# Kernel optimization log

Measured on AMD Instinct MI355X. Metric: run time of the kernel, lower is better.

## Reference

```python
import jax, jax.numpy as jnp
import numpy as np

EMB_DIM = 256
N_EGO = 8192
N_SIDE = 8192
TOP_K = 16


def setup_inputs() -> dict:
    key = jax.random.key(0)
    ks = jax.random.split(key, 9)
    s = 1.0 / np.sqrt(EMB_DIM)
    return {
        "ego_emb": jax.random.normal(ks[0], (N_EGO, EMB_DIM), jnp.float32),
        "side_emb": jax.random.normal(ks[1], (N_SIDE, EMB_DIM), jnp.float32),
        "rel_emb": jax.random.normal(ks[2], (N_SIDE, EMB_DIM), jnp.float32),
        "Wq": jax.random.uniform(ks[3], (EMB_DIM, EMB_DIM), jnp.float32, -s, s),
        "bq": jax.random.uniform(ks[4], (EMB_DIM,), jnp.float32, -s, s),
        "Wk": jax.random.uniform(ks[5], (EMB_DIM, EMB_DIM), jnp.float32, -s, s),
        "bk": jax.random.uniform(ks[6], (EMB_DIM,), jnp.float32, -s, s),
        "Wv": jax.random.uniform(ks[7], (EMB_DIM, EMB_DIM), jnp.float32, -s, s),
        "bv": jax.random.uniform(ks[8], (EMB_DIM,), jnp.float32, -s, s),
    }


def reference(ego_emb, side_emb, rel_emb, Wq, bq, Wk, bk, Wv, bv):
    # Linear projections (torch nn.Linear: x @ W.T + b)
    q = ego_emb @ Wq.T + bq                      # [N_ego, d]
    k = (side_emb * rel_emb) @ Wk.T + bk         # [N_side, d]
    v = side_emb @ Wv.T + bv                     # [N_side, d]

    scale = jnp.sqrt(jnp.asarray(EMB_DIM, q.dtype))
    attn_scores = (q @ k.T) / scale              # [N_ego, N_side] dense

    k_value = min(TOP_K, attn_scores.shape[-1])
    topk_scores, topk_indices = jax.lax.top_k(attn_scores, k_value)  # [N_ego, K]
    attn_weights = jax.nn.softmax(topk_scores, axis=-1)              # [N_ego, K]

    topk_v = v[topk_indices]                     # gather -> [N_ego, K, d]
    aggregated = jnp.sum(topk_v * attn_weights[..., None], axis=1)   # [N_ego, d]
    return aggregated
```

## Files before the change

### kernel.cpp

```cpp
#include <hip/hip_runtime.h>
#include <hip/hip_bf16.h>


#define EMB 256
#define NEGO 8192
#define NSIDE 8192
#define TOPKK 16
#define NSPLIT 8
#define SPLITLEN (NSIDE / NSPLIT)
#define BM 128
#define BN 32
#define NGRP (SPLITLEN / BN)
#define CAP 8
#define RESCORE 20

typedef _Float16 f16x8 __attribute__((ext_vector_type(8)));
typedef float f32x16 __attribute__((ext_vector_type(16)));

#define NEG_BIG (-3.402823466e38f)

__device__ __forceinline__ void gload_lds16(const _Float16* g, _Float16* l) {
    __builtin_amdgcn_global_load_lds((const __attribute__((address_space(1))) void*)g,
                                     (__attribute__((address_space(3))) void*)l, 16, 0, 0);
}

__device__ __forceinline__ void split8(const float* xv, f16x8& hi, f16x8& lo) {
#pragma unroll
    for (int j = 0; j < 8; ++j) {
        float x = xv[j];
        _Float16 h = (_Float16)x;
        hi[j] = h;
        lo[j] = (_Float16)(x - (float)h);
    }
}

__device__ __forceinline__ unsigned packkey(float s, unsigned gid) {
    unsigned b = __float_as_uint(s);
    b = ((int)b >= 0) ? (b | 0x80000000u) : ~b;
    return (b & 0xFFFFE000u) | (gid ^ 0x1FFFu);
}

__global__ __launch_bounds__(256, 1) void proj_kernel(
    const float* __restrict__ ego, const float* __restrict__ side, const float* __restrict__ rel,
    const float* __restrict__ Wq, const float* __restrict__ bq,
    const float* __restrict__ Wk, const float* __restrict__ bk,
    const float* __restrict__ Wv, const float* __restrict__ bv,
    _Float16* __restrict__ qh, _Float16* __restrict__ ql,
    _Float16* __restrict__ kh, _Float16* __restrict__ kl,
    float* __restrict__ vout)
{
    __shared__ __align__(16) _Float16 Wh[64 * 256];
    __shared__ __align__(16) _Float16 Wl[64 * 256];

    const int z = blockIdx.y;
    const float* X; const float* W; const float* bias;
    if (z == 0)      { X = ego;  W = Wq; bias = bq; }
    else if (z == 1) { X = side; W = Wk; bias = bk; }
    else             { X = side; W = Wv; bias = bv; }

    const int tid = threadIdx.x, lane = tid & 63, wave = tid >> 6;
    const int hk = lane >> 5, r = lane & 31;
    const int arow = blockIdx.x * BM + wave * 32 + r;

    f16x8 ah[16], al[16];
#pragma unroll
    for (int kst = 0; kst < 16; ++kst) {
        float xv[8];
        const float* p = X + arow * EMB + kst * 16 + hk * 8;
        const float4 x0 = *(const float4*)p;
        const float4 x1 = *(const float4*)(p + 4);
        xv[0]=x0.x; xv[1]=x0.y; xv[2]=x0.z; xv[3]=x0.w;
        xv[4]=x1.x; xv[5]=x1.y; xv[6]=x1.z; xv[7]=x1.w;
        if (z == 1) {
            const float* pr = rel + arow * EMB + kst * 16 + hk * 8;
            const float4 r0 = *(const float4*)pr;
            const float4 r1 = *(const float4*)(pr + 4);
            xv[0]*=r0.x; xv[1]*=r0.y; xv[2]*=r0.z; xv[3]*=r0.w;
            xv[4]*=r1.x; xv[5]*=r1.y; xv[6]*=r1.z; xv[7]*=r1.w;
        }
        split8(xv, ah[kst], al[kst]);
    }

    for (int nt = 0; nt < 4; ++nt) {
        __syncthreads();
#pragma unroll
        for (int i = 0; i < 8; ++i) {
            const int rowi = wave * 16 + i * 2 + hk;
            const int c = r;
            const float* wp = W + (nt * 64 + rowi) * EMB + ((c ^ (rowi & 31)) << 3);
            float xv[8];
            const float4 w0 = *(const float4*)wp;
            const float4 w1 = *(const float4*)(wp + 4);
            xv[0]=w0.x; xv[1]=w0.y; xv[2]=w0.z; xv[3]=w0.w;
            xv[4]=w1.x; xv[5]=w1.y; xv[6]=w1.z; xv[7]=w1.w;
            f16x8 h8, l8;
            split8(xv, h8, l8);
            *(f16x8*)&Wh[rowi * 256 + c * 8] = h8;
            *(f16x8*)&Wl[rowi * 256 + c * 8] = l8;
        }
        __syncthreads();

        f32x16 acc0 = {}, acc1 = {};
#pragma unroll
        for (int kst = 0; kst < 16; ++kst) {
            const int cc = kst * 2 + hk;
            const f16x8 bh0 = *(const f16x8*)&Wh[r * 256 + ((cc ^ r) << 3)];
            const f16x8 bl0 = *(const f16x8*)&Wl[r * 256 + ((cc ^ r) << 3)];
            const f16x8 bh1 = *(const f16x8*)&Wh[(32 + r) * 256 + ((cc ^ r) << 3)];
            const f16x8 bl1 = *(const f16x8*)&Wl[(32 + r) * 256 + ((cc ^ r) << 3)];
            acc0 = __builtin_amdgcn_mfma_f32_32x32x16_f16(ah[kst], bh0, acc0, 0, 0, 0);
            acc0 = __builtin_amdgcn_mfma_f32_32x32x16_f16(al[kst], bh0, acc0, 0, 0, 0);
            acc0 = __builtin_amdgcn_mfma_f32_32x32x16_f16(ah[kst], bl0, acc0, 0, 0, 0);
            acc1 = __builtin_amdgcn_mfma_f32_32x32x16_f16(ah[kst], bh1, acc1, 0, 0, 0);
            acc1 = __builtin_amdgcn_mfma_f32_32x32x16_f16(al[kst], bh1, acc1, 0, 0, 0);
            acc1 = __builtin_amdgcn_mfma_f32_32x32x16_f16(ah[kst], bl1, acc1, 0, 0, 0);
        }

#pragma unroll
        for (int reg = 0; reg < 16; ++reg) {
            const int crow = (reg & 3) + 8 * (reg >> 2) + 4 * hk;
            const int grow = blockIdx.x * BM + wave * 32 + crow;
            const int col0 = nt * 64 + r;
            const int col1 = nt * 64 + 32 + r;
            const float v0 = acc0[reg] + bias[col0];
            const float v1 = acc1[reg] + bias[col1];
            if (z < 2) {
                _Float16* oh = (z == 0) ? qh : kh;
                _Float16* ol = (z == 0) ? ql : kl;
                _Float16 h0 = (_Float16)v0;
                oh[grow * EMB + col0] = h0;
                ol[grow * EMB + col0] = (_Float16)(v0 - (float)h0);
                _Float16 h1 = (_Float16)v1;
                oh[grow * EMB + col1] = h1;
                ol[grow * EMB + col1] = (_Float16)(v1 - (float)h1);
            } else {
                vout[grow * EMB + col0] = v0;
                vout[grow * EMB + col1] = v1;
            }
        }
    }
}

__global__ __launch_bounds__(256, 2) void scores_topk_kernel(
    const _Float16* __restrict__ qh,
    const _Float16* __restrict__ kh,
    unsigned* __restrict__ part)
{
    __shared__ __align__(16) _Float16 Bh[2 * BN * 256];
    __shared__ unsigned stk[(CAP + 1) * 256];

    const int tid = threadIdx.x, lane = tid & 63, wave = tid >> 6;
    const int hk = lane >> 5, r = lane & 31;
    const int split = blockIdx.x & 7;
    const int bx = blockIdx.x >> 3;
    const int qbase = bx * BM + wave * 32;
    const int rowoff0 = 4 * hk;
    const int gidbase = split * SPLITLEN;

    unsigned tk[16];
    unsigned curmin = 0u;

    f16x8 ah[16];
#pragma unroll
    for (int kst = 0; kst < 16; ++kst) {
        ah[kst] = *(const f16x8*)(qh + (qbase + r) * EMB + kst * 16 + hk * 8);
    }

    auto minTree = [&]() {
        unsigned m0 = min(tk[0], tk[1]),  m1 = min(tk[2], tk[3]);
        unsigned m2 = min(tk[4], tk[5]),  m3 = min(tk[6], tk[7]);
        unsigned m4 = min(tk[8], tk[9]),  m5 = min(tk[10], tk[11]);
        unsigned m6 = min(tk[12], tk[13]), m7 = min(tk[14], tk[15]);
        m0 = min(m0, m1); m2 = min(m2, m3); m4 = min(m4, m5); m6 = min(m6, m7);
        curmin = min(min(m0, m2), min(m4, m6));
    };

    auto insert = [&](unsigned k) {
        const bool p = k > curmin;
        const unsigned target = p ? curmin : 0xFFFFFFFFu;
#pragma unroll
        for (int j = 0; j < 16; ++j) {
            tk[j] = (tk[j] == target) ? k : tk[j];
        }
        minTree();
    };

    int cnt = 0;
    auto rebuild = [&]() {
        int mc = cnt;
#pragma unroll
        for (int o = 32; o; o >>= 1) { const int t = __shfl_xor(mc, o); mc = t > mc ? t : mc; }
        unsigned v = stk[tid];
        for (int e = 0; e < mc; ++e) {
            const unsigned vn = stk[(e + 1) * 256 + tid];
            insert((e < cnt) ? v : 0u);
            v = vn;
        }
        cnt = 0;
    };

#define STAGE(t, b) do {                                                        \
        const int s0_ = gidbase + (t) * BN;                                     \
        _Float16* bh_ = &Bh[(b) * BN * 256];                                    \
        _Pragma("unroll")                                                       \
        for (int i_ = 0; i_ < 4; ++i_) {                                        \
            const int rho0_ = wave * 8 + i_ * 2;                                \
            const int rho_ = rho0_ + hk;                                        \
            const int gsrc_ = (s0_ + rho_) * EMB + ((r ^ (rho_ & 31)) << 3);    \
            gload_lds16(kh + gsrc_, bh_ + rho0_ * 256);                         \
        }                                                                       \
    } while (0)

    STAGE(0, 0);
    __syncthreads();

    for (int gi = 0; gi < NGRP; ++gi) {
        if (gi + 1 < NGRP) STAGE(gi + 1, (gi + 1) & 1);

        const _Float16* bh = &Bh[(gi & 1) * BN * 256];

        f32x16 acc = {};
#pragma unroll
        for (int kst = 0; kst < 16; ++kst) {
            const int slice = kst * 2 + hk;
            const int addr = r * 256 + ((slice ^ r) << 3);
            const f16x8 k_h = *(const f16x8*)&bh[addr];
            acc = __builtin_amdgcn_mfma_f32_32x32x16_f16(k_h, ah[kst], acc, 0, 0, 0);
        }

        if (gi == 0) {
#pragma unroll
            for (int j = 0; j < 16; ++j) {
                const unsigned gid = (unsigned)(gidbase + (j & 3) + 8 * (j >> 2) + rowoff0);
                tk[j] = packkey(acc[j], gid);
            }
            minTree();
        } else {
            const int base_col = gidbase + gi * BN + rowoff0;
#pragma unroll
            for (int h = 0; h < 2; ++h) {
#pragma unroll
                for (int jj = 0; jj < 8; ++jj) {
                    const int j = h * 8 + jj;
                    const unsigned gid = (unsigned)(base_col + (j & 3) + 8 * (j >> 2));
                    const unsigned key = packkey(acc[j], gid);
                    const bool p = key > curmin;
                    stk[cnt * 256 + tid] = key;
                    cnt += p ? 1 : 0;
                }
                if (__any(cnt > 0)) rebuild();
            }
        }

        __syncthreads();
    }
#undef STAGE

    {
        unsigned osv[16];
#pragma unroll
        for (int j = 0; j < 16; ++j) osv[j] = (unsigned)__shfl_xor((int)tk[j], 32);
#pragma unroll
        for (int j = 0; j < 16; ++j) insert(osv[j]);
    }

    if (lane < 32) {
        const int row = qbase + r;
#pragma unroll
        for (int j = 0; j < 16; ++j) {
            part[(row * NSPLIT + split) * TOPKK + j] = tk[j];
        }
    }
}

__global__ __launch_bounds__(256) void merge_kernel(
    const unsigned* __restrict__ part,
    const _Float16* __restrict__ qh, const _Float16* __restrict__ ql,
    const _Float16* __restrict__ kh, const _Float16* __restrict__ kl,
    const float* __restrict__ v, float* __restrict__ out)
{
    __shared__ int   isel[4][RESCORE];
    __shared__ float rsc[4][RESCORE];
    const int tid = threadIdx.x, lane = tid & 63, wave = tid >> 6;
    const int row = blockIdx.x * 4 + wave;

    unsigned c0 = part[row * 128 + lane];
    unsigned c1 = part[row * 128 + 64 + lane];

    for (int t = 0; t < RESCORE; ++t) {
        unsigned bs = c0 > c1 ? c0 : c1;
#pragma unroll
        for (int o = 1; o < 64; o <<= 1) {
            const unsigned os = (unsigned)__shfl_xor((int)bs, o);
            bs = os > bs ? os : bs;
        }
        if (lane == 0) isel[wave][t] = (int)((bs & 0x1FFFu) ^ 0x1FFFu);
        c0 = (c0 == bs) ? 0u : c0;
        c1 = (c1 == bs) ? 0u : c1;
    }
    __syncthreads();

    const int g = lane >> 4, gl = lane & 15;
    float qr[16];
    {
        const f16x8 qa = *(const f16x8*)(qh + (size_t)row * EMB + gl * 16);
        const f16x8 qb = *(const f16x8*)(qh + (size_t)row * EMB + gl * 16 + 8);
        const f16x8 la = *(const f16x8*)(ql + (size_t)row * EMB + gl * 16);
        const f16x8 lb = *(const f16x8*)(ql + (size_t)row * EMB + gl * 16 + 8);
#pragma unroll
        for (int j = 0; j < 8; ++j) {
            qr[j]     = (float)qa[j] + (float)la[j];
            qr[8 + j] = (float)qb[j] + (float)lb[j];
        }
    }

#pragma unroll
    for (int rd = 0; rd < RESCORE / 4; ++rd) {
        const int cidx = rd * 4 + g;
        const int id = isel[wave][cidx];
        const f16x8 ka = *(const f16x8*)(kh + (size_t)id * EMB + gl * 16);
        const f16x8 kb = *(const f16x8*)(kh + (size_t)id * EMB + gl * 16 + 8);
        const f16x8 ma = *(const f16x8*)(kl + (size_t)id * EMB + gl * 16);
        const f16x8 mb = *(const f16x8*)(kl + (size_t)id * EMB + gl * 16 + 8);
        float p = 0.f;
#pragma unroll
        for (int j = 0; j < 8; ++j) {
            p = fmaf(qr[j],     (float)ka[j] + (float)ma[j], p);
            p = fmaf(qr[8 + j], (float)kb[j] + (float)mb[j], p);
        }
#pragma unroll
        for (int o = 1; o < 16; o <<= 1) p += __shfl_xor(p, o);
        if (gl == 0) rsc[wave][cidx] = p;
    }
    __syncthreads();

    float es = (lane < RESCORE) ? rsc[wave][lane] : NEG_BIG;
    int  eid = (lane < RESCORE) ? isel[wave][lane] : 0x7fffffff;
    float w16[16]; int id16[16];
    float m = 0.f, denom = 0.f;
    for (int t = 0; t < 16; ++t) {
        float bs = es; int bid = eid;
#pragma unroll
        for (int o = 1; o < 64; o <<= 1) {
            const float os = __shfl_xor(bs, o);
            const int oid = __shfl_xor(bid, o);
            if (os > bs || (os == bs && oid < bid)) { bs = os; bid = oid; }
        }
        if (t == 0) m = bs;
        if (eid == bid) { es = NEG_BIG; eid = 0x7fffffff; }
        const float e = expf((bs - m) * 0.0625f);
        w16[t] = e; id16[t] = bid; denom += e;
    }
    const float inv = 1.0f / denom;

    float a0 = 0.f, a1 = 0.f, a2 = 0.f, a3 = 0.f;
#pragma unroll
    for (int t = 0; t < 16; ++t) {
        const float w = w16[t] * inv;
        const float* vp = v + (long)id16[t] * EMB;
        a0 += w * vp[lane];
        a1 += w * vp[lane + 64];
        a2 += w * vp[lane + 128];
        a3 += w * vp[lane + 192];
    }
    out[row * EMB + lane]       = a0;
    out[row * EMB + lane + 64]  = a1;
    out[row * EMB + lane + 128] = a2;
    out[row * EMB + lane + 192] = a3;
}

extern "C" void kernel_launch(void* const* d_in, const int* in_sizes, int n_in,
                              void* d_out, int out_size, void* d_ws, size_t ws_size,
                              hipStream_t stream) {
    (void)in_sizes; (void)n_in; (void)out_size; (void)ws_size;
    const float* ego  = (const float*)d_in[0];
    const float* side = (const float*)d_in[1];
    const float* rel  = (const float*)d_in[2];
    const float* Wq   = (const float*)d_in[3];
    const float* bq   = (const float*)d_in[4];
    const float* Wk   = (const float*)d_in[5];
    const float* bk   = (const float*)d_in[6];
    const float* Wv   = (const float*)d_in[7];
    const float* bv   = (const float*)d_in[8];

    char* ws = (char*)d_ws;
    _Float16* qh = (_Float16*)ws;
    _Float16* ql = qh + (size_t)NEGO * EMB;
    _Float16* kh = ql + (size_t)NEGO * EMB;
    _Float16* kl = kh + (size_t)NSIDE * EMB;
    float*    vbuf = (float*)(ws + 16u * 1024 * 1024);
    unsigned* part = (unsigned*)(ws + 24u * 1024 * 1024);
    float* out = (float*)d_out;

    proj_kernel<<<dim3(NEGO / BM, 3), dim3(256), 0, stream>>>(
        ego, side, rel, Wq, bq, Wk, bk, Wv, bv, qh, ql, kh, kl, vbuf);
    scores_topk_kernel<<<dim3(NEGO / BM * NSPLIT), dim3(256), 0, stream>>>(
        qh, kh, part);
    merge_kernel<<<dim3(NEGO / 4), dim3(256), 0, stream>>>(
        part, qh, ql, kh, kl, vbuf, out);
}
```

Before: 200.0 us.

## Double side-split count, drop LDS double buffering, raise occupancy to four blocks

Splits the side dimension into 16 chunks instead of 8, so the grid has twice as many blocks, each doing half the work. The K tile goes from double to single buffered, with a synchronous load and barrier each iteration, which frees LDS for a launch bound of 4 blocks per CU. The merge kernel now reads and reduces 256 candidates per row instead of 128. The cost is that the load-compute overlap is lost, partial-result traffic doubles and merge work grows, all traded for more parallelism and latency hiding from occupancy.

```diff
diff --git a/kernel.cpp b/kernel.cpp
--- a/kernel.cpp
+++ b/kernel.cpp
@@ -6,7 +6,7 @@
 #define NEGO 8192
 #define NSIDE 8192
 #define TOPKK 16
-#define NSPLIT 8
+#define NSPLIT 16
 #define SPLITLEN (NSIDE / NSPLIT)
 #define BM 128
 #define BN 32
@@ -141,18 +141,18 @@
     }
 }
 
-__global__ __launch_bounds__(256, 2) void scores_topk_kernel(
+__global__ __launch_bounds__(256, 4) void scores_topk_kernel(
     const _Float16* __restrict__ qh,
     const _Float16* __restrict__ kh,
     unsigned* __restrict__ part)
 {
-    __shared__ __align__(16) _Float16 Bh[2 * BN * 256];
+    __shared__ __align__(16) _Float16 Bh[BN * 256];
     __shared__ unsigned stk[(CAP + 1) * 256];
 
     const int tid = threadIdx.x, lane = tid & 63, wave = tid >> 6;
     const int hk = lane >> 5, r = lane & 31;
-    const int split = blockIdx.x & 7;
-    const int bx = blockIdx.x >> 3;
+    const int split = blockIdx.x & 15;
+    const int bx = blockIdx.x >> 4;
     const int qbase = bx * BM + wave * 32;
     const int rowoff0 = 4 * hk;
     const int gidbase = split * SPLITLEN;
@@ -199,32 +199,23 @@
         cnt = 0;
     };
 
-#define STAGE(t, b) do {                                                        \
-        const int s0_ = gidbase + (t) * BN;                                     \
-        _Float16* bh_ = &Bh[(b) * BN * 256];                                    \
-        _Pragma("unroll")                                                       \
-        for (int i_ = 0; i_ < 4; ++i_) {                                        \
-            const int rho0_ = wave * 8 + i_ * 2;                                \
-            const int rho_ = rho0_ + hk;                                        \
-            const int gsrc_ = (s0_ + rho_) * EMB + ((r ^ (rho_ & 31)) << 3);    \
-            gload_lds16(kh + gsrc_, bh_ + rho0_ * 256);                         \
-        }                                                                       \
-    } while (0)
-
-    STAGE(0, 0);
-    __syncthreads();
-
     for (int gi = 0; gi < NGRP; ++gi) {
-        if (gi + 1 < NGRP) STAGE(gi + 1, (gi + 1) & 1);
-
-        const _Float16* bh = &Bh[(gi & 1) * BN * 256];
+        const int s0 = gidbase + gi * BN;
+#pragma unroll
+        for (int i = 0; i < 4; ++i) {
+            const int rho0 = wave * 8 + i * 2;
+            const int rho = rho0 + hk;
+            const int gsrc = (s0 + rho) * EMB + ((r ^ (rho & 31)) << 3);
+            gload_lds16(kh + gsrc, &Bh[rho0 * 256]);
+        }
+        __syncthreads();
 
         f32x16 acc = {};
 #pragma unroll
         for (int kst = 0; kst < 16; ++kst) {
             const int slice = kst * 2 + hk;
             const int addr = r * 256 + ((slice ^ r) << 3);
-            const f16x8 k_h = *(const f16x8*)&bh[addr];
+            const f16x8 k_h = *(const f16x8*)&Bh[addr];
             acc = __builtin_amdgcn_mfma_f32_32x32x16_f16(k_h, ah[kst], acc, 0, 0, 0);
         }
 
@@ -251,10 +242,8 @@
                 if (__any(cnt > 0)) rebuild();
             }
         }
-
         __syncthreads();
     }
-#undef STAGE
 
     {
         unsigned osv[16];
@@ -284,11 +273,15 @@
     const int tid = threadIdx.x, lane = tid & 63, wave = tid >> 6;
     const int row = blockIdx.x * 4 + wave;
 
-    unsigned c0 = part[row * 128 + lane];
-    unsigned c1 = part[row * 128 + 64 + lane];
+    unsigned c0 = part[row * 256 + lane];
+    unsigned c1 = part[row * 256 + 64 + lane];
+    unsigned c2 = part[row * 256 + 128 + lane];
+    unsigned c3 = part[row * 256 + 192 + lane];
 
     for (int t = 0; t < RESCORE; ++t) {
         unsigned bs = c0 > c1 ? c0 : c1;
+        const unsigned b2 = c2 > c3 ? c2 : c3;
+        bs = bs > b2 ? bs : b2;
 #pragma unroll
         for (int o = 1; o < 64; o <<= 1) {
             const unsigned os = (unsigned)__shfl_xor((int)bs, o);
@@ -297,6 +290,8 @@
         if (lane == 0) isel[wave][t] = (int)((bs & 0x1FFFu) ^ 0x1FFFu);
         c0 = (c0 == bs) ? 0u : c0;
         c1 = (c1 == bs) ? 0u : c1;
+        c2 = (c2 == bs) ? 0u : c2;
+        c3 = (c3 == bs) ? 0u : c3;
     }
     __syncthreads();
 
```

After: 213.7 us. 6.9% more time.
